# Kernel tuning notes

Hardware: AMD Instinct MI355X
Metric: run time of the kernel (lower is better)

Reference implementation:

```python
import jax, jax.numpy as jnp
import numpy as np

B, N, D_IN, H, L, NH, PE, DEG, OUT = 8, 1024, 128, 256, 4, 8, 8, 16, 1
BN = B * N
E = BN * DEG
DH = H // NH
EPS = 1e-5


def _gelu(x):
    return jax.nn.gelu(x, approximate=False)  # torch nn.GELU default (erf)


def _bn(x, g, b):
    # BatchNorm1d in training mode: batch mean / biased variance over node dim
    m = x.mean(axis=0)
    v = x.var(axis=0)
    return (x - m) * jax.lax.rsqrt(v + EPS) * g + b


def setup_inputs() -> dict:
    key = jax.random.key(0)
    ks = jax.random.split(key, 30)
    s = 0.05
    x = jax.random.normal(ks[0], (BN, D_IN), jnp.float32)
    # block-diagonal COO adjacency: edges stay within each graph's node block
    base = jnp.repeat(jnp.arange(B, dtype=jnp.int32) * N, N * DEG)
    edge_row = base + jax.random.randint(ks[1], (E,), 0, N, jnp.int32)
    edge_col = base + jax.random.randint(ks[2], (E,), 0, N, jnp.int32)
    edge_val = jax.random.uniform(ks[3], (E,), jnp.float32) / DEG
    batch_pe = jax.random.normal(ks[4], (BN, PE), jnp.float32)
    p = {
        'W_in': jax.random.normal(ks[5], (H, D_IN)) * s,
        'b_in': jnp.zeros((H,)),
        'W_pe': jax.random.normal(ks[6], (H, PE)) * s,
        'b_pe': jnp.zeros((H,)),
        'gcn_W': jax.random.normal(ks[7], (L, H, H)) * s,
        'attn_in_W': jax.random.normal(ks[8], (L, 3 * H, H)) * s,
        'attn_in_b': jnp.zeros((L, 3 * H)),
        'attn_out_W': jax.random.normal(ks[9], (L, H, H)) * s,
        'attn_out_b': jnp.zeros((L, H)),
        'bn_g': jnp.ones((L, 3, H)),
        'bn_b': jnp.zeros((L, 3, H)),
        'ffn_W1': jax.random.normal(ks[10], (L, 4 * H, H)) * s,
        'ffn_b1': jnp.zeros((L, 4 * H)),
        'ffn_W2': jax.random.normal(ks[11], (L, H, 4 * H)) * s,
        'ffn_b2': jnp.zeros((L, H)),
        'head_W1': jax.random.normal(ks[12], (H // 2, H)) * s,
        'head_b1': jnp.zeros((H // 2,)),
        'head_W2': jax.random.normal(ks[13], (OUT, H // 2)) * s,
        'head_b2': jnp.zeros((OUT,)),
    }
    p = {k: v.astype(jnp.float32) for k, v in p.items()}
    return dict(x=x, edge_row=edge_row, edge_col=edge_col, edge_val=edge_val,
                batch_pe=batch_pe, **p)


def reference(x, edge_row, edge_col, edge_val, batch_pe,
              W_in, b_in, W_pe, b_pe,
              gcn_W, attn_in_W, attn_in_b, attn_out_W, attn_out_b,
              bn_g, bn_b, ffn_W1, ffn_b1, ffn_W2, ffn_b2,
              head_W1, head_b1, head_W2, head_b2):
    h = x @ W_in.T + b_in + batch_pe @ W_pe.T + b_pe  # (BN, H)
    scale = 1.0 / jnp.sqrt(jnp.asarray(DH, h.dtype))
    for l in range(L):
        # local GCN: linear -> sparse mm (block-diag COO) -> GELU
        msg = edge_val[:, None] * (h @ gcn_W[l].T)[edge_col]  # (E, H)
        h_local = _gelu(jax.ops.segment_sum(msg, edge_row, num_segments=BN))
        h = _bn(h + h_local, bn_g[l, 0], bn_b[l, 0])
        # global self-attention over each graph's N nodes
        hh = h.reshape(B, N, H)
        qkv = hh @ attn_in_W[l].T + attn_in_b[l]  # (B, N, 3H)
        q, k, v = [t.reshape(B, N, NH, DH) for t in jnp.split(qkv, 3, axis=-1)]
        att = jax.nn.softmax(jnp.einsum('bqhd,bkhd->bhqk', q, k) * scale, axis=-1)
        o = jnp.einsum('bhqk,bkhd->bqhd', att, v).reshape(B, N, H)
        o = (o @ attn_out_W[l].T + attn_out_b[l]).reshape(BN, H)
        h = _bn(h + o, bn_g[l, 1], bn_b[l, 1])
        # FFN
        f = _gelu(h @ ffn_W1[l].T + ffn_b1[l]) @ ffn_W2[l].T + ffn_b2[l]
        h = _bn(h + f, bn_g[l, 2], bn_b[l, 2])
    out = jax.nn.sigmoid(_gelu(h @ head_W1.T + head_b1) @ head_W2.T + head_b2)
    return out
```

## Files before the change

kernel.cpp:

```cpp
#include <hip/hip_runtime.h>
#include <hip/hip_bf16.h>
#include <math.h>

#define BB 8
#define NN 1024
#define BN 8192
#define D_IN 128
#define HH 256
#define LL 4
#define NHD 8
#define DH 32
#define EE 131072
#define EPSV 1e-5f

typedef unsigned short u16;
typedef unsigned int u32;
typedef __attribute__((ext_vector_type(8))) short bf16x8;
typedef __attribute__((ext_vector_type(4))) float f32x4;

__device__ __forceinline__ float gelu_erf(float x) {
    return 0.5f * x * (1.0f + erff(x * 0.70710678118654752f));
}

__device__ __forceinline__ u16 f2bf(float v) {
    __hip_bfloat16 b = __float2bfloat16(v);
    return *reinterpret_cast<u16*>(&b);
}

__device__ __forceinline__ float bf2f(u16 u) {
    u32 x = ((u32)u) << 16;
    return __builtin_bit_cast(float, x);
}

__device__ __forceinline__ u32 pack2bf(float lo, float hi) {
    return ((u32)f2bf(hi) << 16) | (u32)f2bf(lo);
}

__global__ __launch_bounds__(256) void cast_all_kernel(
        const float* s0, const float* s1, const float* s2, const float* s3,
        const float* s4, const float* s5, const float* s6, const float* s7,
        u16* d0, u16* d1, u16* d2, u16* d3, u16* d4, u16* d5, u16* d6, u16* d7) {
    int blk = blockIdx.x;
    const float* s; u16* d; int base;
    if      (blk < 1024) { s = s0; d = d0; base = 0; }
    else if (blk < 1056) { s = s1; d = d1; base = 1024; }
    else if (blk < 1312) { s = s2; d = d2; base = 1056; }
    else if (blk < 2080) { s = s3; d = d3; base = 1312; }
    else if (blk < 2336) { s = s4; d = d4; base = 2080; }
    else if (blk < 3360) { s = s5; d = d5; base = 2336; }
    else if (blk < 4384) { s = s6; d = d6; base = 3360; }
    else                 { s = s7; d = d7; base = 4384; }
    int i = (blk - base) * 256 + threadIdx.x;
    float4 v = ((const float4*)s)[i];
    ushort4 o;
    o.x = f2bf(v.x); o.y = f2bf(v.y); o.z = f2bf(v.z); o.w = f2bf(v.w);
    ((ushort4*)d)[i] = o;
}

__global__ __launch_bounds__(256) void hist_kernel(const int* __restrict__ edge_row,
                                                   int* __restrict__ counts) {
    int e = blockIdx.x * 256 + threadIdx.x;
    atomicAdd(&counts[edge_row[e]], 1);
}

__global__ __launch_bounds__(256) void prefix_kernel(const int* __restrict__ counts,
                                                     int* __restrict__ row_start,
                                                     int* __restrict__ cursor) {
    __shared__ int lds[256];
    int t = threadIdx.x;
    int local[32];
    int s = 0;
#pragma unroll
    for (int i = 0; i < 32; ++i) { local[i] = counts[t * 32 + i]; s += local[i]; }
    lds[t] = s;
    __syncthreads();
    for (int off = 1; off < 256; off <<= 1) {
        int v = (t >= off) ? lds[t - off] : 0;
        __syncthreads();
        lds[t] += v;
        __syncthreads();
    }
    int excl = (t == 0) ? 0 : lds[t - 1];
#pragma unroll
    for (int i = 0; i < 32; ++i) {
        int c = local[i];
        row_start[t * 32 + i] = excl;
        cursor[t * 32 + i] = excl;
        excl += c;
    }
    if (t == 255) row_start[8192] = excl;
}

__global__ __launch_bounds__(256) void scatter_kernel(const int* __restrict__ edge_row,
                                                      int* __restrict__ cursor,
                                                      int* __restrict__ csr_e) {
    int e = blockIdx.x * 256 + threadIdx.x;
    int r = edge_row[e];
    int pos = atomicAdd(&cursor[r], 1);
    csr_e[pos] = e;
}

__global__ __launch_bounds__(256) void gcn_gather_kernel(const u16* __restrict__ t1b,
                                                         const int* __restrict__ row_start,
                                                         const int* __restrict__ csr_e,
                                                         const int* __restrict__ edge_col,
                                                         const float* __restrict__ edge_val,
                                                         float* __restrict__ outb) {
    int wave = threadIdx.x >> 6;
    int lane = threadIdx.x & 63;
    int r = blockIdx.x * 4 + wave;
    float a0 = 0.f, a1 = 0.f, a2 = 0.f, a3 = 0.f;
    int p0 = row_start[r], p1 = row_start[r + 1];
    for (int p = p0; p < p1; ++p) {
        int e = csr_e[p];
        int c = edge_col[e];
        float v = edge_val[e];
        ushort4 sv = *(const ushort4*)&t1b[(size_t)c * HH + lane * 4];
        a0 += v * bf2f(sv.x); a1 += v * bf2f(sv.y);
        a2 += v * bf2f(sv.z); a3 += v * bf2f(sv.w);
    }
    float4 g;
    g.x = gelu_erf(a0); g.y = gelu_erf(a1); g.z = gelu_erf(a2); g.w = gelu_erf(a3);
    *(float4*)&outb[(size_t)r * HH + lane * 4] = g;
}

__global__ __launch_bounds__(256) void bn_reduce_kernel(float* __restrict__ h,
                                                        const float* __restrict__ add,
                                                        float* __restrict__ psum,
                                                        float* __restrict__ psq) {
    int c = threadIdx.x;
    int chunk = blockIdx.x;
    int r0 = chunk * 32;
    float s = 0.f, q = 0.f;
#pragma unroll 4
    for (int i = 0; i < 32; ++i) {
        int idx = (r0 + i) * HH + c;
        float v = h[idx] + add[idx];
        h[idx] = v;
        s += v; q += v * v;
    }
    psum[chunk * HH + c] = s;
    psq[chunk * HH + c] = q;
}

__global__ __launch_bounds__(256) void bn_finalize_kernel(const float* __restrict__ psum,
                                                          const float* __restrict__ psq,
                                                          const float* __restrict__ g,
                                                          const float* __restrict__ b,
                                                          float* __restrict__ scale,
                                                          float* __restrict__ shift) {
    __shared__ float ls[16][17], lq[16][17];
    int t = threadIdx.x;
    int cl = t & 15, grp = t >> 4;
    int c = blockIdx.x * 16 + cl;
    float s = 0.f, q = 0.f;
#pragma unroll
    for (int i = 0; i < 16; ++i) {
        int chunk = grp * 16 + i;
        s += psum[chunk * HH + c];
        q += psq[chunk * HH + c];
    }
    ls[grp][cl] = s; lq[grp][cl] = q;
    __syncthreads();
    if (t < 16) {
        float ss = 0.f, qq = 0.f;
#pragma unroll
        for (int gg = 0; gg < 16; ++gg) { ss += ls[gg][t]; qq += lq[gg][t]; }
        int ch = blockIdx.x * 16 + t;
        float mean = ss * (1.f / 8192.f);
        float var = qq * (1.f / 8192.f) - mean * mean;
        float sc = g[ch] * rsqrtf(var + EPSV);
        scale[ch] = sc;
        shift[ch] = b[ch] - mean * sc;
    }
}

__global__ __launch_bounds__(256) void bn_apply_kernel(float* __restrict__ h,
                                                       u16* __restrict__ hb,
                                                       const float* __restrict__ scale,
                                                       const float* __restrict__ shift) {
    int i = blockIdx.x * 256 + threadIdx.x;
    float4 v = ((float4*)h)[i];
    int c4 = (i & 63) * 4;
    v.x = v.x * scale[c4 + 0] + shift[c4 + 0];
    v.y = v.y * scale[c4 + 1] + shift[c4 + 1];
    v.z = v.z * scale[c4 + 2] + shift[c4 + 2];
    v.w = v.w * scale[c4 + 3] + shift[c4 + 3];
    ((float4*)h)[i] = v;
    ushort4 o;
    o.x = f2bf(v.x); o.y = f2bf(v.y); o.z = f2bf(v.z); o.w = f2bf(v.w);
    ((ushort4*)hb)[i] = o;
}

#define SWZ(row, c8) ((c8) ^ (((row) & 7) << 3))
template <int EPI, int OUTBF>
__global__ __launch_bounds__(256) void gemm_mfma(const u16* __restrict__ A,
                                                 const u16* __restrict__ W,
                                                 const float* __restrict__ bias,
                                                 void* __restrict__ Cout,
                                                 int M, int K, int N) {
    __shared__ u16 As[128][64];
    __shared__ u16 Ws[64][64];
    int t = threadIdx.x;
    int bm = blockIdx.y * 128, bn = blockIdx.x * 64;
    int wid = t >> 6, lane = t & 63;
    int wr = wid >> 1, wc = wid & 1;
    int lr = lane & 15, lg = lane >> 4;

    f32x4 zero = {0.f, 0.f, 0.f, 0.f};
    f32x4 acc[4][2];
#pragma unroll
    for (int mi = 0; mi < 4; ++mi)
#pragma unroll
        for (int ni = 0; ni < 2; ++ni) acc[mi][ni] = zero;

    int sr = t >> 3;
    int c8 = (t & 7) * 8;

    for (int k0 = 0; k0 < K; k0 += 64) {
        __syncthreads();
#pragma unroll
        for (int p = 0; p < 4; ++p) {
            int row = sr + p * 32;
            const u16* src = A + (size_t)(bm + row) * K + k0 + c8;
            *(int4*)&As[row][SWZ(row, c8)] = *(const int4*)src;
        }
#pragma unroll
        for (int p = 0; p < 2; ++p) {
            int row = sr + p * 32;
            const u16* src = W + (size_t)(bn + row) * K + k0 + c8;
            *(int4*)&Ws[row][SWZ(row, c8)] = *(const int4*)src;
        }
        __syncthreads();
#pragma unroll
        for (int kk = 0; kk < 2; ++kk) {
            bf16x8 af[4], bf[2];
#pragma unroll
            for (int mi = 0; mi < 4; ++mi) {
                int row = wr * 64 + mi * 16 + lr;
                af[mi] = *(const bf16x8*)&As[row][SWZ(row, kk * 32 + lg * 8)];
            }
#pragma unroll
            for (int ni = 0; ni < 2; ++ni) {
                int row = wc * 32 + ni * 16 + lr;
                bf[ni] = *(const bf16x8*)&Ws[row][SWZ(row, kk * 32 + lg * 8)];
            }
#pragma unroll
            for (int mi = 0; mi < 4; ++mi)
#pragma unroll
                for (int ni = 0; ni < 2; ++ni)
                    acc[mi][ni] = __builtin_amdgcn_mfma_f32_16x16x32_bf16(af[mi], bf[ni], acc[mi][ni], 0, 0, 0);
        }
    }

#pragma unroll
    for (int ni = 0; ni < 2; ++ni) {
        int col = bn + wc * 32 + ni * 16 + lr;
        float bj = bias ? bias[col] : 0.f;
#pragma unroll
        for (int mi = 0; mi < 4; ++mi) {
#pragma unroll
            for (int r = 0; r < 4; ++r) {
                int row = bm + wr * 64 + mi * 16 + lg * 4 + r;
                float v = acc[mi][ni][r] + bj;
                if (EPI == 1) v = gelu_erf(v);
                if (OUTBF)
                    ((u16*)Cout)[(size_t)row * N + col] = f2bf(v);
                else
                    ((float*)Cout)[(size_t)row * N + col] = v;
            }
        }
    }
}

template <int EPI, int OUTBF>
__global__ __launch_bounds__(256) void gemm_mfma2(const u16* __restrict__ A,
                                                  const u16* __restrict__ W,
                                                  const float* __restrict__ bias,
                                                  void* __restrict__ Cout,
                                                  int M, int K, int N) {
    __shared__ u16 As[128][64];
    __shared__ u16 Ws[128][64];
    int t = threadIdx.x;
    int bm = blockIdx.y * 128, bn = blockIdx.x * 128;
    int wid = t >> 6, lane = t & 63;
    int wr = wid >> 1, wc = wid & 1;
    int lr = lane & 15, lg = lane >> 4;

    f32x4 zero = {0.f, 0.f, 0.f, 0.f};
    f32x4 acc[4][4];
#pragma unroll
    for (int mi = 0; mi < 4; ++mi)
#pragma unroll
        for (int ni = 0; ni < 4; ++ni) acc[mi][ni] = zero;

    int sr = t >> 3;
    int c8 = (t & 7) * 8;

    for (int k0 = 0; k0 < K; k0 += 64) {
        __syncthreads();
#pragma unroll
        for (int p = 0; p < 4; ++p) {
            int row = sr + p * 32;
            const u16* srcA = A + (size_t)(bm + row) * K + k0 + c8;
            *(int4*)&As[row][SWZ(row, c8)] = *(const int4*)srcA;
            const u16* srcW = W + (size_t)(bn + row) * K + k0 + c8;
            *(int4*)&Ws[row][SWZ(row, c8)] = *(const int4*)srcW;
        }
        __syncthreads();
#pragma unroll
        for (int kk = 0; kk < 2; ++kk) {
            bf16x8 af[4], bf[4];
#pragma unroll
            for (int mi = 0; mi < 4; ++mi) {
                int row = wr * 64 + mi * 16 + lr;
                af[mi] = *(const bf16x8*)&As[row][SWZ(row, kk * 32 + lg * 8)];
            }
#pragma unroll
            for (int ni = 0; ni < 4; ++ni) {
                int row = wc * 64 + ni * 16 + lr;
                bf[ni] = *(const bf16x8*)&Ws[row][SWZ(row, kk * 32 + lg * 8)];
            }
#pragma unroll
            for (int mi = 0; mi < 4; ++mi)
#pragma unroll
                for (int ni = 0; ni < 4; ++ni)
                    acc[mi][ni] = __builtin_amdgcn_mfma_f32_16x16x32_bf16(af[mi], bf[ni], acc[mi][ni], 0, 0, 0);
        }
    }

#pragma unroll
    for (int ni = 0; ni < 4; ++ni) {
        int col = bn + wc * 64 + ni * 16 + lr;
        float bj = bias ? bias[col] : 0.f;
#pragma unroll
        for (int mi = 0; mi < 4; ++mi) {
#pragma unroll
            for (int r = 0; r < 4; ++r) {
                int row = bm + wr * 64 + mi * 16 + lg * 4 + r;
                float v = acc[mi][ni][r] + bj;
                if (EPI == 1) v = gelu_erf(v);
                if (OUTBF)
                    ((u16*)Cout)[(size_t)row * N + col] = f2bf(v);
                else
                    ((float*)Cout)[(size_t)row * N + col] = v;
            }
        }
    }
}

__global__ __launch_bounds__(256) void pe_add_kernel(const float* __restrict__ pe,
                                                     const float* __restrict__ Wpe,
                                                     const float* __restrict__ bpe,
                                                     float* __restrict__ h,
                                                     u16* __restrict__ hb) {
    __shared__ float Ws[256][9];
    int t = threadIdx.x;
    for (int i = t; i < 2048; i += 256) Ws[i >> 3][i & 7] = Wpe[i];
    __syncthreads();
    int r = blockIdx.x;
    int c = t;
    float s = bpe[c];
    const float* pr = pe + r * 8;
#pragma unroll
    for (int k = 0; k < 8; ++k) s += pr[k] * Ws[c][k];
    float nv = h[(size_t)r * HH + c] + s;
    h[(size_t)r * HH + c] = nv;
    hb[(size_t)r * HH + c] = f2bf(nv);
}

__global__ __launch_bounds__(256) void vtrans_kernel(const u16* __restrict__ qkv,
                                                     u16* __restrict__ vT) {
    __shared__ u16 Ls[64][64];
    int bid = blockIdx.x;
    int kt = bid & 15;
    int head = (bid >> 4) & 7;
    int b = bid >> 7;
    int t = threadIdx.x;
    int key_l = t >> 2, blkS = t & 3;
    const u16* src = qkv + (size_t)(b * NN + kt * 64 + key_l) * 768 + 512 + head * DH + blkS * 8;
    int sb = (blkS ^ (key_l & 7) ^ ((key_l >> 3) & 7)) * 8;
    *(int4*)&Ls[key_l][sb] = *(const int4*)src;
    __syncthreads();
    int d = t >> 3, kc = t & 7;
    union { u16 a[8]; int4 v; } tmp;
#pragma unroll
    for (int j = 0; j < 8; ++j) {
        int col = (((d >> 3) ^ j ^ kc) << 3) | (d & 7);
        tmp.a[j] = Ls[kc * 8 + j][col];
    }
    u16* dst = vT + (size_t)((b * 8 + head) * 32 + d) * NN + kt * 64 + kc * 8;
    *(int4*)dst = tmp.v;
}

__global__ __launch_bounds__(256) void attn_mfma_kernel(const u16* __restrict__ qkv,
                                                        const u16* __restrict__ vT,
                                                        u16* __restrict__ o) {
    __shared__ __align__(16) u16 Ks[64][40];
    __shared__ __align__(16) u16 Vt[32][72];
    __shared__ __align__(16) u16 Ot[64][40];
    int bid = blockIdx.x;
    int qt = bid & 15;
    int head = (bid >> 4) & 7;
    int b = bid >> 7;
    int t = threadIdx.x;
    int w = t >> 6, lane = t & 63;
    int lr = lane & 15, lg = lane >> 4;

    bf16x8 qf;
    {
        const u16* qsrc = qkv + (size_t)(b * NN + qt * 64 + w * 16 + lr) * 768 + head * DH + lg * 8;
        bf16x8 raw = *(const bf16x8*)qsrc;
#pragma unroll
        for (int j = 0; j < 8; ++j) {
            float f = bf2f((u16)raw[j]) * 0.17677669529663689f;
            qf[j] = (short)f2bf(f);
        }
    }

    f32x4 zero = {0.f, 0.f, 0.f, 0.f};
    f32x4 oacc[2] = {zero, zero};
    float m = -1e30f, l = 0.f;

    int srow = t >> 2, sc8 = (t & 3) * 8;
    int vd = t >> 3, vc8 = (t & 7) * 8;
    const u16* kbase = qkv + (size_t)(b * NN) * 768 + 256 + head * DH + sc8;
    const u16* vbase = vT + (size_t)((b * 8 + head) * 32 + vd) * NN + vc8;

    int srcA = ((lg & 1) << 5) + lr;
    int srcB = srcA + 16;
    int hi = lg >> 1;

    for (int k0 = 0; k0 < NN; k0 += 64) {
        __syncthreads();
        *(int4*)&Ks[srow][sc8] = *(const int4*)(kbase + (size_t)(k0 + srow) * 768);
        *(int4*)&Vt[vd][vc8] = *(const int4*)(vbase + k0);
        __syncthreads();

        f32x4 st[4];
#pragma unroll
        for (int kt = 0; kt < 4; ++kt) {
            bf16x8 kf = *(const bf16x8*)&Ks[kt * 16 + lr][lg * 8];
            st[kt] = __builtin_amdgcn_mfma_f32_16x16x32_bf16(kf, qf, zero, 0, 0, 0);
        }

        float tm = -1e30f;
#pragma unroll
        for (int kt = 0; kt < 4; ++kt)
#pragma unroll
            for (int r = 0; r < 4; ++r) tm = fmaxf(tm, st[kt][r]);
        tm = fmaxf(tm, __shfl_xor(tm, 16));
        tm = fmaxf(tm, __shfl_xor(tm, 32));
        float mn = fmaxf(m, tm);
        float corr = __expf(m - mn);
        l *= corr;
#pragma unroll
        for (int dh = 0; dh < 2; ++dh)
#pragma unroll
            for (int r = 0; r < 4; ++r) oacc[dh][r] *= corr;

        float ps = 0.f;
        u32 pw0[4], pw1[4];
#pragma unroll
        for (int kt = 0; kt < 4; ++kt) {
            float p0 = __expf(st[kt][0] - mn);
            float p1 = __expf(st[kt][1] - mn);
            float p2 = __expf(st[kt][2] - mn);
            float p3 = __expf(st[kt][3] - mn);
            ps += (p0 + p1) + (p2 + p3);
            pw0[kt] = pack2bf(p0, p1);
            pw1[kt] = pack2bf(p2, p3);
        }
        ps += __shfl_xor(ps, 16);
        ps += __shfl_xor(ps, 32);
        l += ps;
        m = mn;

#pragma unroll
        for (int c = 0; c < 2; ++c) {
            u32 w0a = (u32)__shfl((int)pw0[c * 2], srcA);
            u32 w0b = (u32)__shfl((int)pw0[c * 2 + 1], srcA);
            u32 w1a = (u32)__shfl((int)pw1[c * 2], srcA);
            u32 w1b = (u32)__shfl((int)pw1[c * 2 + 1], srcA);
            u32 w2a = (u32)__shfl((int)pw0[c * 2], srcB);
            u32 w2b = (u32)__shfl((int)pw0[c * 2 + 1], srcB);
            u32 w3a = (u32)__shfl((int)pw1[c * 2], srcB);
            u32 w3b = (u32)__shfl((int)pw1[c * 2 + 1], srcB);
            union { bf16x8 v; u32 u[4]; } pf;
            pf.u[0] = hi ? w0b : w0a;
            pf.u[1] = hi ? w1b : w1a;
            pf.u[2] = hi ? w2b : w2a;
            pf.u[3] = hi ? w3b : w3a;
#pragma unroll
            for (int dh = 0; dh < 2; ++dh) {
                bf16x8 vf = *(const bf16x8*)&Vt[dh * 16 + lr][c * 32 + lg * 8];
                oacc[dh] = __builtin_amdgcn_mfma_f32_16x16x32_bf16(vf, pf.v, oacc[dh], 0, 0, 0);
            }
        }
    }

    float inv = 1.f / l;
    __syncthreads();
#pragma unroll
    for (int dh = 0; dh < 2; ++dh)
#pragma unroll
        for (int r = 0; r < 4; ++r)
            Ot[w * 16 + lr][dh * 16 + lg * 4 + r] = f2bf(oacc[dh][r] * inv);
    __syncthreads();
    {
        int orow = t >> 2, oc8 = (t & 3) * 8;
        u16* dst = o + (size_t)(b * NN + qt * 64 + orow) * HH + head * DH + oc8;
        *(int4*)dst = *(const int4*)&Ot[orow][oc8];
    }
}

__global__ __launch_bounds__(256) void head2_kernel(const float* __restrict__ g1,
                                                    const float* __restrict__ W2,
                                                    const float* __restrict__ b2,
                                                    float* __restrict__ out) {
    __shared__ float w[128];
    int t = threadIdx.x;
    if (t < 128) w[t] = W2[t];
    __syncthreads();
    int r = blockIdx.x * 256 + t;
    float s = b2[0];
    const float* row = g1 + (size_t)r * 128;
#pragma unroll
    for (int k = 0; k < 128; k += 4) {
        float4 v = *(const float4*)&row[k];
        s += v.x * w[k] + v.y * w[k + 1] + v.z * w[k + 2] + v.w * w[k + 3];
    }
    out[r] = 1.f / (1.f + __expf(-s));
}

extern "C" void kernel_launch(void* const* d_in, const int* in_sizes, int n_in,
                              void* d_out, int out_size, void* d_ws, size_t ws_size,
                              hipStream_t stream) {
    const float* x        = (const float*)d_in[0];
    const int*   edge_row = (const int*)d_in[1];
    const int*   edge_col = (const int*)d_in[2];
    const float* edge_val = (const float*)d_in[3];
    const float* pe       = (const float*)d_in[4];
    const float* W_in     = (const float*)d_in[5];
    const float* b_in     = (const float*)d_in[6];
    const float* W_pe     = (const float*)d_in[7];
    const float* b_pe     = (const float*)d_in[8];
    const float* gcn_W    = (const float*)d_in[9];
    const float* attn_in_W  = (const float*)d_in[10];
    const float* attn_in_b  = (const float*)d_in[11];
    const float* attn_out_W = (const float*)d_in[12];
    const float* attn_out_b = (const float*)d_in[13];
    const float* bn_g     = (const float*)d_in[14];
    const float* bn_b     = (const float*)d_in[15];
    const float* ffn_W1   = (const float*)d_in[16];
    const float* ffn_b1   = (const float*)d_in[17];
    const float* ffn_W2   = (const float*)d_in[18];
    const float* ffn_b2   = (const float*)d_in[19];
    const float* head_W1  = (const float*)d_in[20];
    const float* head_b1  = (const float*)d_in[21];
    const float* head_W2  = (const float*)d_in[22];
    const float* head_b2  = (const float*)d_in[23];
    float* out = (float*)d_out;

    float* w = (float*)d_ws;
    float* h    = w; w += 2097152;
    float* buf1 = w; w += 8388608;
    float* buf2 = w; w += 2097152;
    float* buf3 = w; w += 2097152;
    float* psum = w; w += 65536;
    float* psq  = w; w += 65536;
    float* scale = w; w += 256;
    float* shift = w; w += 256;
    int* counts    = (int*)w; w += 8192;
    int* row_start = (int*)w; w += 8224;
    int* cursor    = (int*)w; w += 8192;
    int* csr_e     = (int*)w; w += 131072;
    u16* hb   = (u16*)w;
    u16* xb   = hb + 2097152;
    u16* aob  = xb + 1048576;
    u16* wbWin = aob + 2097152;
    u16* wbGcn = wbWin + 32768;
    u16* wbAin = wbGcn + 262144;
    u16* wbAout = wbAin + 786432;
    u16* wbF1  = wbAout + 262144;
    u16* wbF2  = wbF1 + 1048576;
    u16* wbH1  = wbF2 + 1048576;
    u16* t1b  = (u16*)buf1;
    u16* qkvb = (u16*)buf1;
    u16* midb = (u16*)buf1;
    u16* vT   = (u16*)buf1 + 12582912;

    hipMemsetAsync(counts, 0, 8192 * sizeof(int), stream);
    hist_kernel<<<512, 256, 0, stream>>>(edge_row, counts);
    prefix_kernel<<<1, 256, 0, stream>>>(counts, row_start, cursor);
    scatter_kernel<<<512, 256, 0, stream>>>(edge_row, cursor, csr_e);

    cast_all_kernel<<<4416, 256, 0, stream>>>(
        x, W_in, gcn_W, attn_in_W, attn_out_W, ffn_W1, ffn_W2, head_W1,
        xb, wbWin, wbGcn, wbAin, wbAout, wbF1, wbF2, wbH1);

    gemm_mfma<0, 0><<<dim3(4, 64), 256, 0, stream>>>(xb, wbWin, b_in, h, BN, D_IN, HH);
    pe_add_kernel<<<BN, 256, 0, stream>>>(pe, W_pe, b_pe, h, hb);

    for (int l = 0; l < LL; ++l) {
        gemm_mfma<0, 1><<<dim3(4, 64), 256, 0, stream>>>(hb, wbGcn + l * 65536, nullptr, t1b, BN, HH, HH);
        gcn_gather_kernel<<<2048, 256, 0, stream>>>(t1b, row_start, csr_e, edge_col, edge_val, buf2);
        bn_reduce_kernel<<<256, 256, 0, stream>>>(h, buf2, psum, psq);
        bn_finalize_kernel<<<16, 256, 0, stream>>>(psum, psq, bn_g + (l * 3 + 0) * 256, bn_b + (l * 3 + 0) * 256, scale, shift);
        bn_apply_kernel<<<2048, 256, 0, stream>>>(h, hb, scale, shift);

        gemm_mfma2<0, 1><<<dim3(6, 64), 256, 0, stream>>>(hb, wbAin + l * 196608, attn_in_b + l * 768, qkvb, BN, HH, 768);
        vtrans_kernel<<<1024, 256, 0, stream>>>(qkvb, vT);
        attn_mfma_kernel<<<1024, 256, 0, stream>>>(qkvb, vT, aob);
        gemm_mfma<0, 0><<<dim3(4, 64), 256, 0, stream>>>(aob, wbAout + l * 65536, attn_out_b + l * 256, buf3, BN, HH, HH);
        bn_reduce_kernel<<<256, 256, 0, stream>>>(h, buf3, psum, psq);
        bn_finalize_kernel<<<16, 256, 0, stream>>>(psum, psq, bn_g + (l * 3 + 1) * 256, bn_b + (l * 3 + 1) * 256, scale, shift);
        bn_apply_kernel<<<2048, 256, 0, stream>>>(h, hb, scale, shift);

        gemm_mfma2<1, 1><<<dim3(8, 64), 256, 0, stream>>>(hb, wbF1 + l * 262144, ffn_b1 + l * 1024, midb, BN, HH, 1024);
        gemm_mfma<0, 0><<<dim3(4, 64), 256, 0, stream>>>(midb, wbF2 + l * 262144, ffn_b2 + l * 256, buf2, BN, 1024, HH);
        bn_reduce_kernel<<<256, 256, 0, stream>>>(h, buf2, psum, psq);
        bn_finalize_kernel<<<16, 256, 0, stream>>>(psum, psq, bn_g + (l * 3 + 2) * 256, bn_b + (l * 3 + 2) * 256, scale, shift);
        bn_apply_kernel<<<2048, 256, 0, stream>>>(h, hb, scale, shift);
    }

    gemm_mfma<1, 0><<<dim3(2, 64), 256, 0, stream>>>(hb, wbH1, head_b1, buf1, BN, HH, 128);
    head2_kernel<<<32, 256, 0, stream>>>(buf1, head_W2, head_b2, out);
}
```

Baseline: 844.3 us.

## Fuse residual add and BN statistics into GEMM epilogues with atomic accumulation

Replaces the per-chunk partial sums and the separate finalize kernel with atomic accumulation of per-channel sums into double-buffered stat arrays. Mean, variance, scale and shift are now computed inside the apply kernel, which also zeroes the next stage's buffers. For the attention-out and FFN2 GEMMs, the residual add and the stat accumulation move into the GEMM epilogue, which removes the reduce kernels and the intermediate buffer round trips. The PE add kernel is also vectorised to one wave per row. In exchange, the atomics make the summation order nondeterministic, and the apply kernel now recomputes the per-channel statistics in every thread.

Result: no change. 847.4 us (+0.4%).

```diff
diff --git a/kernel.cpp b/kernel.cpp
--- a/kernel.cpp
+++ b/kernel.cpp
@@ -124,13 +124,12 @@
     *(float4*)&outb[(size_t)r * HH + lane * 4] = g;
 }
 
-__global__ __launch_bounds__(256) void bn_reduce_kernel(float* __restrict__ h,
-                                                        const float* __restrict__ add,
-                                                        float* __restrict__ psum,
-                                                        float* __restrict__ psq) {
+__global__ __launch_bounds__(256) void bn_reduce_atomic_kernel(float* __restrict__ h,
+                                                               const float* __restrict__ add,
+                                                               float* __restrict__ S,
+                                                               float* __restrict__ Q) {
     int c = threadIdx.x;
-    int chunk = blockIdx.x;
-    int r0 = chunk * 32;
+    int r0 = blockIdx.x * 32;
     float s = 0.f, q = 0.f;
 #pragma unroll 4
     for (int i = 0; i < 32; ++i) {
@@ -139,66 +138,66 @@
         h[idx] = v;
         s += v; q += v * v;
     }
-    psum[chunk * HH + c] = s;
-    psq[chunk * HH + c] = q;
-}
-
-__global__ __launch_bounds__(256) void bn_finalize_kernel(const float* __restrict__ psum,
-                                                          const float* __restrict__ psq,
-                                                          const float* __restrict__ g,
-                                                          const float* __restrict__ b,
-                                                          float* __restrict__ scale,
-                                                          float* __restrict__ shift) {
-    __shared__ float ls[16][17], lq[16][17];
-    int t = threadIdx.x;
-    int cl = t & 15, grp = t >> 4;
-    int c = blockIdx.x * 16 + cl;
-    float s = 0.f, q = 0.f;
-#pragma unroll
-    for (int i = 0; i < 16; ++i) {
-        int chunk = grp * 16 + i;
-        s += psum[chunk * HH + c];
-        q += psq[chunk * HH + c];
-    }
-    ls[grp][cl] = s; lq[grp][cl] = q;
-    __syncthreads();
-    if (t < 16) {
-        float ss = 0.f, qq = 0.f;
-#pragma unroll
-        for (int gg = 0; gg < 16; ++gg) { ss += ls[gg][t]; qq += lq[gg][t]; }
-        int ch = blockIdx.x * 16 + t;
-        float mean = ss * (1.f / 8192.f);
-        float var = qq * (1.f / 8192.f) - mean * mean;
-        float sc = g[ch] * rsqrtf(var + EPSV);
-        scale[ch] = sc;
-        shift[ch] = b[ch] - mean * sc;
-    }
+    atomicAdd(&S[c], s);
+    atomicAdd(&Q[c], q);
 }
 
 __global__ __launch_bounds__(256) void bn_apply_kernel(float* __restrict__ h,
                                                        u16* __restrict__ hb,
-                                                       const float* __restrict__ scale,
-                                                       const float* __restrict__ shift) {
+                                                       const float* __restrict__ S,
+                                                       const float* __restrict__ Q,
+                                                       const float* __restrict__ g,
+                                                       const float* __restrict__ b,
+                                                       float* __restrict__ Zs,
+                                                       float* __restrict__ Zq) {
     int i = blockIdx.x * 256 + threadIdx.x;
     float4 v = ((float4*)h)[i];
     int c4 = (i & 63) * 4;
-    v.x = v.x * scale[c4 + 0] + shift[c4 + 0];
-    v.y = v.y * scale[c4 + 1] + shift[c4 + 1];
-    v.z = v.z * scale[c4 + 2] + shift[c4 + 2];
-    v.w = v.w * scale[c4 + 3] + shift[c4 + 3];
-    ((float4*)h)[i] = v;
+    float o0, o1, o2, o3;
+    {
+        float mean = S[c4 + 0] * (1.f / 8192.f);
+        float var = Q[c4 + 0] * (1.f / 8192.f) - mean * mean;
+        float sc = g[c4 + 0] * rsqrtf(var + EPSV);
+        o0 = v.x * sc + (b[c4 + 0] - mean * sc);
+    }
+    {
+        float mean = S[c4 + 1] * (1.f / 8192.f);
+        float var = Q[c4 + 1] * (1.f / 8192.f) - mean * mean;
+        float sc = g[c4 + 1] * rsqrtf(var + EPSV);
+        o1 = v.y * sc + (b[c4 + 1] - mean * sc);
+    }
+    {
+        float mean = S[c4 + 2] * (1.f / 8192.f);
+        float var = Q[c4 + 2] * (1.f / 8192.f) - mean * mean;
+        float sc = g[c4 + 2] * rsqrtf(var + EPSV);
+        o2 = v.z * sc + (b[c4 + 2] - mean * sc);
+    }
+    {
+        float mean = S[c4 + 3] * (1.f / 8192.f);
+        float var = Q[c4 + 3] * (1.f / 8192.f) - mean * mean;
+        float sc = g[c4 + 3] * rsqrtf(var + EPSV);
+        o3 = v.w * sc + (b[c4 + 3] - mean * sc);
+    }
+    float4 ov; ov.x = o0; ov.y = o1; ov.z = o2; ov.w = o3;
+    ((float4*)h)[i] = ov;
     ushort4 o;
-    o.x = f2bf(v.x); o.y = f2bf(v.y); o.z = f2bf(v.z); o.w = f2bf(v.w);
+    o.x = f2bf(o0); o.y = f2bf(o1); o.z = f2bf(o2); o.w = f2bf(o3);
     ((ushort4*)hb)[i] = o;
+    if (blockIdx.x == 0) {
+        Zs[threadIdx.x] = 0.f;
+        Zq[threadIdx.x] = 0.f;
+    }
 }
 
 #define SWZ(row, c8) ((c8) ^ (((row) & 7) << 3))
-template <int EPI, int OUTBF>
+template <int EPI, int OUTMODE>
 __global__ __launch_bounds__(256) void gemm_mfma(const u16* __restrict__ A,
                                                  const u16* __restrict__ W,
                                                  const float* __restrict__ bias,
                                                  void* __restrict__ Cout,
-                                                 int M, int K, int N) {
+                                                 int M, int K, int N,
+                                                 float* __restrict__ psumF,
+                                                 float* __restrict__ psqF) {
     __shared__ u16 As[128][64];
     __shared__ u16 Ws[64][64];
     int t = threadIdx.x;
@@ -253,21 +252,47 @@
         }
     }
 
-#pragma unroll
-    for (int ni = 0; ni < 2; ++ni) {
-        int col = bn + wc * 32 + ni * 16 + lr;
-        float bj = bias ? bias[col] : 0.f;
-#pragma unroll
-        for (int mi = 0; mi < 4; ++mi) {
-#pragma unroll
-            for (int r = 0; r < 4; ++r) {
-                int row = bm + wr * 64 + mi * 16 + lg * 4 + r;
-                float v = acc[mi][ni][r] + bj;
-                if (EPI == 1) v = gelu_erf(v);
-                if (OUTBF)
-                    ((u16*)Cout)[(size_t)row * N + col] = f2bf(v);
-                else
-                    ((float*)Cout)[(size_t)row * N + col] = v;
+    if (OUTMODE == 2) {
+#pragma unroll
+        for (int ni = 0; ni < 2; ++ni) {
+            int col = bn + wc * 32 + ni * 16 + lr;
+            float bj = bias[col];
+            float s = 0.f, q = 0.f;
+#pragma unroll
+            for (int mi = 0; mi < 4; ++mi) {
+#pragma unroll
+                for (int r = 0; r < 4; ++r) {
+                    int row = bm + wr * 64 + mi * 16 + lg * 4 + r;
+                    float* hp = (float*)Cout + (size_t)row * N + col;
+                    float nv = *hp + acc[mi][ni][r] + bj;
+                    *hp = nv;
+                    s += nv; q += nv * nv;
+                }
+            }
+            s += __shfl_xor(s, 16); s += __shfl_xor(s, 32);
+            q += __shfl_xor(q, 16); q += __shfl_xor(q, 32);
+            if (lg == 0) {
+                atomicAdd(&psumF[col], s);
+                atomicAdd(&psqF[col], q);
+            }
+        }
+    } else {
+#pragma unroll
+        for (int ni = 0; ni < 2; ++ni) {
+            int col = bn + wc * 32 + ni * 16 + lr;
+            float bj = bias ? bias[col] : 0.f;
+#pragma unroll
+            for (int mi = 0; mi < 4; ++mi) {
+#pragma unroll
+                for (int r = 0; r < 4; ++r) {
+                    int row = bm + wr * 64 + mi * 16 + lg * 4 + r;
+                    float v = acc[mi][ni][r] + bj;
+                    if (EPI == 1) v = gelu_erf(v);
+                    if (OUTMODE == 1)
+                        ((u16*)Cout)[(size_t)row * N + col] = f2bf(v);
+                    else
+                        ((float*)Cout)[(size_t)row * N + col] = v;
+                }
             }
         }
     }
@@ -354,19 +379,32 @@
                                                      const float* __restrict__ bpe,
                                                      float* __restrict__ h,
                                                      u16* __restrict__ hb) {
-    __shared__ float Ws[256][9];
+    __shared__ float Ws[8][256];
     int t = threadIdx.x;
-    for (int i = t; i < 2048; i += 256) Ws[i >> 3][i & 7] = Wpe[i];
+    for (int i = t; i < 2048; i += 256) Ws[i & 7][i >> 3] = Wpe[i];
     __syncthreads();
-    int r = blockIdx.x;
-    int c = t;
-    float s = bpe[c];
+    int w = t >> 6, lane = t & 63;
+    int r = blockIdx.x * 4 + w;
     const float* pr = pe + r * 8;
-#pragma unroll
-    for (int k = 0; k < 8; ++k) s += pr[k] * Ws[c][k];
-    float nv = h[(size_t)r * HH + c] + s;
-    h[(size_t)r * HH + c] = nv;
-    hb[(size_t)r * HH + c] = f2bf(nv);
+    float p[8];
+#pragma unroll
+    for (int k = 0; k < 8; ++k) p[k] = pr[k];
+    int c0 = lane * 4;
+    float4 hv = *(float4*)&h[(size_t)r * HH + c0];
+    float o0 = hv.x + bpe[c0 + 0], o1 = hv.y + bpe[c0 + 1];
+    float o2 = hv.z + bpe[c0 + 2], o3 = hv.w + bpe[c0 + 3];
+#pragma unroll
+    for (int k = 0; k < 8; ++k) {
+        o0 += p[k] * Ws[k][c0 + 0];
+        o1 += p[k] * Ws[k][c0 + 1];
+        o2 += p[k] * Ws[k][c0 + 2];
+        o3 += p[k] * Ws[k][c0 + 3];
+    }
+    float4 ov; ov.x = o0; ov.y = o1; ov.z = o2; ov.w = o3;
+    *(float4*)&h[(size_t)r * HH + c0] = ov;
+    ushort4 ob;
+    ob.x = f2bf(o0); ob.y = f2bf(o1); ob.z = f2bf(o2); ob.w = f2bf(o3);
+    *(ushort4*)&hb[(size_t)r * HH + c0] = ob;
 }
 
 __global__ __launch_bounds__(256) void vtrans_kernel(const u16* __restrict__ qkv,
@@ -566,12 +604,8 @@
     float* h    = w; w += 2097152;
     float* buf1 = w; w += 8388608;
     float* buf2 = w; w += 2097152;
-    float* buf3 = w; w += 2097152;
-    float* psum = w; w += 65536;
-    float* psq  = w; w += 65536;
-    float* scale = w; w += 256;
-    float* shift = w; w += 256;
     int* counts    = (int*)w; w += 8192;
+    float* bnstats = w; w += 1024;
     int* row_start = (int*)w; w += 8224;
     int* cursor    = (int*)w; w += 8192;
     int* csr_e     = (int*)w; w += 131072;
@@ -590,7 +624,10 @@
     u16* midb = (u16*)buf1;
     u16* vT   = (u16*)buf1 + 12582912;
 
-    hipMemsetAsync(counts, 0, 8192 * sizeof(int), stream);
+    auto Sp = [&](int k) { return bnstats + (k & 1) * 512; };
+    auto Qp = [&](int k) { return bnstats + (k & 1) * 512 + 256; };
+
+    hipMemsetAsync(counts, 0, (8192 + 1024) * sizeof(int), stream);
     hist_kernel<<<512, 256, 0, stream>>>(edge_row, counts);
     prefix_kernel<<<1, 256, 0, stream>>>(counts, row_start, cursor);
     scatter_kernel<<<512, 256, 0, stream>>>(edge_row, cursor, csr_e);
@@ -599,31 +636,31 @@
         x, W_in, gcn_W, attn_in_W, attn_out_W, ffn_W1, ffn_W2, head_W1,
         xb, wbWin, wbGcn, wbAin, wbAout, wbF1, wbF2, wbH1);
 
-    gemm_mfma<0, 0><<<dim3(4, 64), 256, 0, stream>>>(xb, wbWin, b_in, h, BN, D_IN, HH);
-    pe_add_kernel<<<BN, 256, 0, stream>>>(pe, W_pe, b_pe, h, hb);
+    gemm_mfma<0, 0><<<dim3(4, 64), 256, 0, stream>>>(xb, wbWin, b_in, h, BN, D_IN, HH, bnstats, bnstats);
+    pe_add_kernel<<<2048, 256, 0, stream>>>(pe, W_pe, b_pe, h, hb);
 
     for (int l = 0; l < LL; ++l) {
-        gemm_mfma<0, 1><<<dim3(4, 64), 256, 0, stream>>>(hb, wbGcn + l * 65536, nullptr, t1b, BN, HH, HH);
+        int k1 = l * 3, k2 = l * 3 + 1, k3 = l * 3 + 2;
+
+        gemm_mfma<0, 1><<<dim3(4, 64), 256, 0, stream>>>(hb, wbGcn + l * 65536, nullptr, t1b, BN, HH, HH, bnstats, bnstats);
         gcn_gather_kernel<<<2048, 256, 0, stream>>>(t1b, row_start, csr_e, edge_col, edge_val, buf2);
-        bn_reduce_kernel<<<256, 256, 0, stream>>>(h, buf2, psum, psq);
-        bn_finalize_kernel<<<16, 256, 0, stream>>>(psum, psq, bn_g + (l * 3 + 0) * 256, bn_b + (l * 3 + 0) * 256, scale, shift);
-        bn_apply_kernel<<<2048, 256, 0, stream>>>(h, hb, scale, shift);
+        bn_reduce_atomic_kernel<<<256, 256, 0, stream>>>(h, buf2, Sp(k1), Qp(k1));
+        bn_apply_kernel<<<2048, 256, 0, stream>>>(h, hb, Sp(k1), Qp(k1),
+            bn_g + (l * 3 + 0) * 256, bn_b + (l * 3 + 0) * 256, Sp(k1 + 1), Qp(k1 + 1));
 
         gemm_mfma2<0, 1><<<dim3(6, 64), 256, 0, stream>>>(hb, wbAin + l * 196608, attn_in_b + l * 768, qkvb, BN, HH, 768);
         vtrans_kernel<<<1024, 256, 0, stream>>>(qkvb, vT);
         attn_mfma_kernel<<<1024, 256, 0, stream>>>(qkvb, vT, aob);
-        gemm_mfma<0, 0><<<dim3(4, 64), 256, 0, stream>>>(aob, wbAout + l * 65536, attn_out_b + l * 256, buf3, BN, HH, HH);
-        bn_reduce_kernel<<<256, 256, 0, stream>>>(h, buf3, psum, psq);
-        bn_finalize_kernel<<<16, 256, 0, stream>>>(psum, psq, bn_g + (l * 3 + 1) * 256, bn_b + (l * 3 + 1) * 256, scale, shift);
-        bn_apply_kernel<<<2048, 256, 0, stream>>>(h, hb, scale, shift);
+        gemm_mfma<0, 2><<<dim3(4, 64), 256, 0, stream>>>(aob, wbAout + l * 65536, attn_out_b + l * 256, h, BN, HH, HH, Sp(k2), Qp(k2));
+        bn_apply_kernel<<<2048, 256, 0, stream>>>(h, hb, Sp(k2), Qp(k2),
+            bn_g + (l * 3 + 1) * 256, bn_b + (l * 3 + 1) * 256, Sp(k2 + 1), Qp(k2 + 1));
 
         gemm_mfma2<1, 1><<<dim3(8, 64), 256, 0, stream>>>(hb, wbF1 + l * 262144, ffn_b1 + l * 1024, midb, BN, HH, 1024);
-        gemm_mfma<0, 0><<<dim3(4, 64), 256, 0, stream>>>(midb, wbF2 + l * 262144, ffn_b2 + l * 256, buf2, BN, 1024, HH);
-        bn_reduce_kernel<<<256, 256, 0, stream>>>(h, buf2, psum, psq);
-        bn_finalize_kernel<<<16, 256, 0, stream>>>(psum, psq, bn_g + (l * 3 + 2) * 256, bn_b + (l * 3 + 2) * 256, scale, shift);
-        bn_apply_kernel<<<2048, 256, 0, stream>>>(h, hb, scale, shift);
-    }
-
-    gemm_mfma<1, 0><<<dim3(2, 64), 256, 0, stream>>>(hb, wbH1, head_b1, buf1, BN, HH, 128);
+        gemm_mfma<0, 2><<<dim3(4, 64), 256, 0, stream>>>(midb, wbF2 + l * 262144, ffn_b2 + l * 256, h, BN, 1024, HH, Sp(k3), Qp(k3));
+        bn_apply_kernel<<<2048, 256, 0, stream>>>(h, hb, Sp(k3), Qp(k3),
+            bn_g + (l * 3 + 2) * 256, bn_b + (l * 3 + 2) * 256, Sp(k3 + 1), Qp(k3 + 1));
+    }
+
+    gemm_mfma<1, 0><<<dim3(2, 64), 256, 0, stream>>>(hb, wbH1, head_b1, buf1, BN, HH, 128, bnstats, bnstats);
     head2_kernel<<<32, 256, 0, stream>>>(buf1, head_W2, head_b2, out);
 }
```
